# Kernel tuning notes

Measured on AMD Instinct MI355X. Metric: run time of the kernel, lower is better.

## Reference

```python
import jax, jax.numpy as jnp
import numpy as np

N = 100_000      # lidar points (KITTI-scale)
E = 800_000      # knn edges, avg degree 8
C_IN = 4
INTERNAL_H, INTERNAL_W = 240, 1216   # INTERNAL_IMG_SIZE


def setup_inputs() -> dict:
    key = jax.random.key(0)
    ks = jax.random.split(key, 16)
    x = jax.random.normal(ks[0], (N, C_IN), jnp.float32)
    # lidar-like points in velodyne frame: x fwd [5,70], y left [-20,20], z up [-2,1]
    u = jax.random.uniform(ks[1], (N, 3), jnp.float32)
    pos = jnp.stack([5.0 + 65.0 * u[:, 0],
                     -20.0 + 40.0 * u[:, 1],
                     -2.0 + 3.0 * u[:, 2]], axis=1)
    edge_index = jax.random.randint(ks[2], (2, E), 0, N, dtype=jnp.int32)
    batch = jnp.zeros((N,), jnp.int32)
    # folded calibration P2 @ R0 @ Tr: pinhole cam looking down velodyne +x
    f, cx, cy = 720.0, 621.0, 250.0
    proj = jnp.array([[cx, -f, 0.0, 0.0],
                      [cy, 0.0, -f, 0.0],
                      [1.0, 0.0, 0.0, 0.0]], jnp.float32)
    dims = [(C_IN + 3, 64), (64 + 3, 128), (128 + 3, 256)]
    params = {}
    ki = 3
    for li, (din, dout) in enumerate(dims, 1):
        s1, s2 = 1.0 / np.sqrt(din), 1.0 / np.sqrt(dout)
        params[f"w1_{li}"] = jax.random.uniform(ks[ki], (din, dout), jnp.float32, -s1, s1); ki += 1
        params[f"b1_{li}"] = jnp.zeros((dout,), jnp.float32)
        params[f"w2_{li}"] = jax.random.uniform(ks[ki], (dout, dout), jnp.float32, -s2, s2); ki += 1
        params[f"b2_{li}"] = jnp.zeros((dout,), jnp.float32)
    return dict(x=x, pos=pos, edge_index=edge_index, batch=batch, proj=proj,
                img_h=375, img_w=1242, **params)


def _pointnet_conv(x, pos, src, dst, w1, b1, w2, b2):
    # message: local_nn([x_j, pos_j - pos_i]) with MLP = lin1 -> relu -> lin2; aggr = max
    m = jnp.concatenate([x[src], pos[src] - pos[dst]], axis=1)     # [E', din]
    h = jnp.maximum(m @ w1 + b1, 0.0) @ w2 + b2                    # [E', dout]
    return jax.ops.segment_max(h, dst, num_segments=x.shape[0])


def reference(x, pos, edge_index, batch, proj, img_h, img_w,
              w1_1, b1_1, w2_1, b2_1,
              w1_2, b1_2, w2_2, b2_2,
              w1_3, b1_3, w2_3, b2_3):
    n = x.shape[0]
    # PointNetConv adds self-loops by default -> every segment non-empty
    loops = jnp.arange(n, dtype=edge_index.dtype)
    src = jnp.concatenate([edge_index[0], loops])
    dst = jnp.concatenate([edge_index[1], loops])

    h = _pointnet_conv(x, pos, src, dst, w1_1, b1_1, w2_1, b2_1)   # [N, 64]
    h = _pointnet_conv(h, pos, src, dst, w1_2, b1_2, w2_2, b2_2)   # [N, 128]
    h = _pointnet_conv(h, pos, src, dst, w1_3, b1_3, w2_3, b2_3)   # [N, 256]

    # projection: (proj @ [pos; 1]) -> [3, N]; perspective divide; int16 trunc
    hom = proj @ jnp.concatenate([pos.T, jnp.ones((1, n), pos.dtype)], axis=0)
    off_u, off_v = img_w - INTERNAL_W, img_h - INTERNAL_H
    ui = (hom[0] / hom[2]).astype(jnp.int16).astype(jnp.int32) - off_u
    vi = (hom[1] / hom[2]).astype(jnp.int16).astype(jnp.int32) - off_v
    valid = (ui >= 0) & (vi >= 0) & (ui < INTERNAL_W) & (vi < INTERNAL_H)
    # route invalid points out-of-bounds so mode='drop' discards them
    ui = jnp.where(valid, ui, INTERNAL_W)
    vi = jnp.where(valid, vi, INTERNAL_H)

    img = jnp.zeros((1, h.shape[1], INTERNAL_W, INTERNAL_H), h.dtype)  # (B=1, C, 1216, 240)
    img = img.at[0, :, ui, vi].add(h, mode='drop')

    # max_pool2d(kernel=4, stride=4) -> (1, 256, 304, 60)
    B, C, W, H = img.shape
    pooled = img.reshape(B, C, W // 4, 4, H // 4, 4).max(axis=(3, 5))
    return pooled
```

## Files before the change

### kernel.cpp

```cpp
#include <hip/hip_runtime.h>
#include <cstdint>

#define N_PTS 100000
#define N_EDGE 800000
#define N_ITEMS (N_EDGE + N_PTS)
#define IMG_W 1216
#define IMG_H 240
#define OW 304
#define OH 60
#define CHUNK 32
#define BIN_BLOCKS 391

typedef _Float16 f16;
typedef _Float16 f16x8 __attribute__((ext_vector_type(8)));
typedef float f32x4 __attribute__((ext_vector_type(4)));

__device__ __forceinline__ void atomicMaxF(float* addr, float v) {
    if (v >= 0.0f) atomicMax((int*)addr, __float_as_int(v));
    else atomicMin((unsigned int*)addr, __float_as_uint(v));
}

__global__ __launch_bounds__(256)
void init_out_kernel(float* __restrict__ p, long n)
{
    long i = ((long)blockIdx.x * 256 + threadIdx.x) * 4;
    if (i < n) {
        float4 v = {-INFINITY, -INFINITY, -INFINITY, -INFINITY};
        *(float4*)&p[i] = v;
    }
}

template<int DX, int KP, int D>
__global__ __launch_bounds__(256)
void node_mfma_kernel(const float* __restrict__ X, const float* __restrict__ pos,
                      const f16* __restrict__ w1t, const float* __restrict__ b1,
                      f16* __restrict__ A)
{
    constexpr int KB = KP / 32;
    constexpr int NB = D / 16;
    const int tid = threadIdx.x;
    const int wave = tid >> 6;
    const int lane = tid & 63;
    const int row = lane & 15;
    const int kg = lane >> 4;
    const int wbase = (blockIdx.x * 4 + wave) * 32;

    f16x8 pa[2][KB];
#pragma unroll
    for (int mh = 0; mh < 2; ++mh) {
        int n = wbase + mh * 16 + row;
        int ns = (n < N_PTS) ? n : 0;
#pragma unroll
        for (int kb = 0; kb < KB; ++kb) {
            const int c0 = kb * 32 + kg * 8;
            f16x8 h;
#pragma unroll
            for (int j = 0; j < 8; ++j) {
                int k = c0 + j;
                float v = 0.0f;
                if (k < DX) v = X[(long)ns * DX + k];
                else if (k < DX + 3) v = pos[(long)ns * 3 + (k - DX)];
                h[j] = (f16)v;
            }
            pa[mh][kb] = h;
        }
    }

#pragma unroll 2
    for (int nb = 0; nb < NB; ++nb) {
        f32x4 acc0 = {0.0f, 0.0f, 0.0f, 0.0f};
        f32x4 acc1 = {0.0f, 0.0f, 0.0f, 0.0f};
#pragma unroll
        for (int kb = 0; kb < KB; ++kb) {
            f16x8 pb = *(const f16x8*)&w1t[(long)(nb * 16 + row) * KP + kb * 32 + kg * 8];
            acc0 = __builtin_amdgcn_mfma_f32_16x16x32_f16(pa[0][kb], pb, acc0, 0, 0, 0);
            acc1 = __builtin_amdgcn_mfma_f32_16x16x32_f16(pa[1][kb], pb, acc1, 0, 0, 0);
        }
        const int col = nb * 16 + row;
        const float bb = b1[col];
#pragma unroll
        for (int reg = 0; reg < 4; ++reg) {
            int r = kg * 4 + reg;
            int n0 = wbase + r;
            int n1 = wbase + 16 + r;
            if (n0 < N_PTS) A[(long)n0 * D + col] = (f16)(acc0[reg] + bb);
            if (n1 < N_PTS) A[(long)n1 * D + col] = (f16)(acc1[reg] + bb);
        }
    }
}

__global__ void cvt_w1(const float* __restrict__ w1, f16* __restrict__ w1t,
                       int K, int KP, int D)
{
    int i = blockIdx.x * 256 + threadIdx.x;
    if (i >= D * KP) return;
    int c = i / KP, k = i % KP;
    w1t[i] = (k < K) ? (f16)w1[k * D + c] : (f16)0.0f;
}

__global__ void cvt_w2(const float* __restrict__ w2, f16* __restrict__ w2t, int D)
{
    int i = blockIdx.x * 256 + threadIdx.x;
    if (i >= D * D) return;
    int n = i / D, k = i % D;
    w2t[i] = (f16)w2[k * D + n];
}

__global__ void init_hist_kernel(int* __restrict__ hist)
{
    int i = blockIdx.x * 256 + threadIdx.x;
    if (i < N_PTS) hist[i] = 1;
}

__global__ void hist_kernel(const int* __restrict__ ei, int* __restrict__ hist)
{
    int e = blockIdx.x * 256 + threadIdx.x;
    if (e < N_EDGE) atomicAdd(&hist[ei[N_EDGE + e]], 1);
}

__global__ void bsum_kernel(const int* __restrict__ hist, int* __restrict__ bsum)
{
    __shared__ int s[256];
    int i = blockIdx.x * 256 + threadIdx.x;
    s[threadIdx.x] = (i < N_PTS) ? hist[i] : 0;
    __syncthreads();
    for (int off = 128; off > 0; off >>= 1) {
        if (threadIdx.x < off) s[threadIdx.x] += s[threadIdx.x + off];
        __syncthreads();
    }
    if (threadIdx.x == 0) bsum[blockIdx.x] = s[0];
}

__global__ void scan_bsum_kernel(int* __restrict__ bsum)
{
    __shared__ int s[512];
    int t = threadIdx.x;
    int v = (t < BIN_BLOCKS) ? bsum[t] : 0;
    s[t] = v;
    __syncthreads();
    for (int off = 1; off < 512; off <<= 1) {
        int u = (t >= off) ? s[t - off] : 0;
        __syncthreads();
        s[t] += u;
        __syncthreads();
    }
    if (t < BIN_BLOCKS) bsum[t] = s[t] - v;
}

__global__ void rowptr_kernel(const int* __restrict__ hist, const int* __restrict__ bsum,
                              int* __restrict__ woff)
{
    __shared__ int s[256];
    int i = blockIdx.x * 256 + threadIdx.x;
    int v = (i < N_PTS) ? hist[i] : 0;
    s[threadIdx.x] = v;
    __syncthreads();
    for (int off = 1; off < 256; off <<= 1) {
        int u = (threadIdx.x >= off) ? s[threadIdx.x - off] : 0;
        __syncthreads();
        s[threadIdx.x] += u;
        __syncthreads();
    }
    if (i < N_PTS) woff[i] = bsum[blockIdx.x] + s[threadIdx.x] - v;
}

__global__ void scatter_edges_kernel(const int* __restrict__ ei, int* __restrict__ woff,
                                     int* __restrict__ srcS, int* __restrict__ dstS)
{
    int e = blockIdx.x * 256 + threadIdx.x;
    if (e >= N_ITEMS) return;
    int s, d;
    if (e < N_EDGE) { s = ei[e]; d = ei[N_EDGE + e]; }
    else            { s = d = e - N_EDGE; }
    int p = atomicAdd(&woff[d], 1);
    srcS[p] = s;
    dstS[p] = d;
}

template<int D>
__global__ __launch_bounds__(256)
void gemm_msg_kernel(const int* __restrict__ srcA, const int* __restrict__ dstA,
                     const f16* __restrict__ A, const float* __restrict__ pos,
                     const float* __restrict__ w1p, const f16* __restrict__ w2t,
                     const float* __restrict__ b2, float* __restrict__ OUT, int nItems)
{
    constexpr int KB = D / 32;
    constexpr int NB = D / 16;
    const int tid = threadIdx.x;
    const int wave = tid >> 6;
    const int lane = tid & 63;
    const int row = lane & 15;
    const int kg = lane >> 4;
    const long wbase = ((long)blockIdx.x * 4 + wave) * 32;

    int s[2], d[2];
    float px[2], py[2], pz[2];
#pragma unroll
    for (int mh = 0; mh < 2; ++mh) {
        long e = wbase + mh * 16 + row;
        bool ok = (e < nItems);
        int ss = ok ? srcA[e] : 0;
        int dd = ok ? dstA[e] : -1;
        s[mh] = ss; d[mh] = dd;
        int dsafe = ok ? dd : 0;
        px[mh] = pos[(long)dsafe * 3 + 0];
        py[mh] = pos[(long)dsafe * 3 + 1];
        pz[mh] = pos[(long)dsafe * 3 + 2];
    }

    f16x8 pa[2][KB];
#pragma unroll
    for (int kb = 0; kb < KB; ++kb) {
        const int c0 = kb * 32 + kg * 8;
        f16x8 a0 = *(const f16x8*)&A[(long)s[0] * D + c0];
        f16x8 a1 = *(const f16x8*)&A[(long)s[1] * D + c0];
        f16x8 h0, h1;
#pragma unroll
        for (int j = 0; j < 8; ++j) {
            float wx = w1p[c0 + j];
            float wy = w1p[D + c0 + j];
            float wz = w1p[2 * D + c0 + j];
            h0[j] = (f16)fmaxf((float)a0[j] - (px[0] * wx + py[0] * wy + pz[0] * wz), 0.0f);
            h1[j] = (f16)fmaxf((float)a1[j] - (px[1] * wx + py[1] * wy + pz[1] * wz), 0.0f);
        }
        pa[0][kb] = h0;
        pa[1][kb] = h1;
    }

    int dd0[4], dd1[4];
#pragma unroll
    for (int reg = 0; reg < 4; ++reg) {
        int r = kg * 4 + reg;
        dd0[reg] = __shfl(d[0], r);
        dd1[reg] = __shfl(d[1], r);
    }
    bool hd0[4], hd1[4];
    hd0[0] = true; hd1[0] = true;
#pragma unroll
    for (int reg = 1; reg < 4; ++reg) {
        hd0[reg] = (dd0[reg] != dd0[reg - 1]);
        hd1[reg] = (dd1[reg] != dd1[reg - 1]);
    }

#pragma unroll
    for (int nb = 0; nb < NB; ++nb) {
        f32x4 acc0 = {0.0f, 0.0f, 0.0f, 0.0f};
        f32x4 acc1 = {0.0f, 0.0f, 0.0f, 0.0f};
#pragma unroll
        for (int kb = 0; kb < KB; ++kb) {
            f16x8 pb = *(const f16x8*)&w2t[(long)(nb * 16 + row) * D + kb * 32 + kg * 8];
            acc0 = __builtin_amdgcn_mfma_f32_16x16x32_f16(pa[0][kb], pb, acc0, 0, 0, 0);
            acc1 = __builtin_amdgcn_mfma_f32_16x16x32_f16(pa[1][kb], pb, acc1, 0, 0, 0);
        }
        const int col = nb * 16 + row;
        const float bb = b2[col];
        float v0[4], v1[4];
#pragma unroll
        for (int reg = 0; reg < 4; ++reg) { v0[reg] = acc0[reg] + bb; v1[reg] = acc1[reg] + bb; }
        float s0[4], s1[4];
        s0[3] = v0[3]; s1[3] = v1[3];
#pragma unroll
        for (int reg = 2; reg >= 0; --reg) {
            s0[reg] = hd0[reg + 1] ? v0[reg] : fmaxf(v0[reg], s0[reg + 1]);
            s1[reg] = hd1[reg + 1] ? v1[reg] : fmaxf(v1[reg], s1[reg + 1]);
        }
#pragma unroll
        for (int reg = 0; reg < 4; ++reg) {
            if (hd0[reg] && dd0[reg] >= 0) atomicMaxF(&OUT[(long)dd0[reg] * D + col], s0[reg]);
            if (hd1[reg] && dd1[reg] >= 0) atomicMaxF(&OUT[(long)dd1[reg] * D + col], s1[reg]);
        }
    }
}

__global__ void proj_kernel(const float* __restrict__ pos, const float* __restrict__ proj,
                            const int* __restrict__ img_h, const int* __restrict__ img_w,
                            int* __restrict__ pix)
{
    int n = blockIdx.x * blockDim.x + threadIdx.x;
    if (n >= N_PTS) return;
    float px = pos[n * 3 + 0], py = pos[n * 3 + 1], pz = pos[n * 3 + 2];
    float h0 = proj[0] * px + proj[1] * py + proj[2]  * pz + proj[3];
    float h1 = proj[4] * px + proj[5] * py + proj[6]  * pz + proj[7];
    float h2 = proj[8] * px + proj[9] * py + proj[10] * pz + proj[11];
    int off_u = img_w[0] - IMG_W;
    int off_v = img_h[0] - IMG_H;
    int ui = (int)(short)(h0 / h2) - off_u;
    int vi = (int)(short)(h1 / h2) - off_v;
    bool valid = (ui >= 0) && (vi >= 0) && (ui < IMG_W) && (vi < IMG_H);
    pix[n] = valid ? (ui * IMG_H + vi) : -1;
}

__global__ __launch_bounds__(256)
void scatter_kernel(const float* __restrict__ H, const int* __restrict__ pix,
                    float* __restrict__ img, int cbase)
{
    long g = (long)blockIdx.x * blockDim.x + threadIdx.x;
    if (g >= (long)N_PTS * CHUNK) return;
    int n = (int)(g / CHUNK);
    int c = (int)(g % CHUNK);
    int p = pix[n];
    if (p < 0) return;
    atomicAdd(&img[(long)p * CHUNK + c], H[(long)n * 256 + cbase + c]);
}

__global__ __launch_bounds__(CHUNK)
void pool_kernel(const float* __restrict__ img, float* __restrict__ out, int cbase)
{
    int cell = blockIdx.x;
    int wc = cell / OH, hc = cell % OH;
    int c = threadIdx.x;
    float mx = -INFINITY;
#pragma unroll
    for (int i = 0; i < 4; ++i)
#pragma unroll
        for (int j = 0; j < 4; ++j) {
            long p = (long)(wc * 4 + i) * IMG_H + (hc * 4 + j);
            mx = fmaxf(mx, img[p * CHUNK + c]);
        }
    out[(long)(cbase + c) * (OW * OH) + wc * OH + hc] = mx;
}

extern "C" void kernel_launch(void* const* d_in, const int* in_sizes, int n_in,
                              void* d_out, int out_size, void* d_ws, size_t ws_size,
                              hipStream_t stream)
{
    const float* x     = (const float*)d_in[0];
    const float* pos   = (const float*)d_in[1];
    const int*   ei    = (const int*)d_in[2];
    const float* proj  = (const float*)d_in[4];
    const int*   img_h = (const int*)d_in[5];
    const int*   img_w = (const int*)d_in[6];
    const float* w1_1 = (const float*)d_in[7];
    const float* b1_1 = (const float*)d_in[8];
    const float* w2_1 = (const float*)d_in[9];
    const float* b2_1 = (const float*)d_in[10];
    const float* w1_2 = (const float*)d_in[11];
    const float* b1_2 = (const float*)d_in[12];
    const float* w2_2 = (const float*)d_in[13];
    const float* b2_2 = (const float*)d_in[14];
    const float* w1_3 = (const float*)d_in[15];
    const float* b1_3 = (const float*)d_in[16];
    const float* w2_3 = (const float*)d_in[17];
    const float* b2_3 = (const float*)d_in[18];
    float* out = (float*)d_out;

    if (ws_size < 162400000ull) return;
    char* ws = (char*)d_ws;
    float* HH   = (float*)(ws + 0);
    float* F1   = (float*)(ws + 0);
    float* F0   = (float*)(ws + 51200000);
    f16*   A12  = (f16*)(ws + 76800000);
    f16*   A3   = (f16*)(ws + 102400000);
    float* img  = (float*)(ws + 102400000);
    int*   pix  = (int*)(ws + 153600000);
    f16*   w2t3 = (f16*)(ws + 154000000);
    f16*   w2t2 = (f16*)(ws + 154131072);
    f16*   w2t1 = (f16*)(ws + 154163840);
    int*   srcS = (int*)(ws + 154200000);
    int*   dstS = (int*)(ws + 157800000);
    int*   hist = (int*)(ws + 161400000);
    int*   woff = (int*)(ws + 161800000);
    int*   bsum = (int*)(ws + 162200000);
    f16*   w1t3 = (f16*)(ws + 162210000);
    f16*   w1t2 = (f16*)(ws + 162300000);
    f16*   w1t1 = (f16*)(ws + 162330000);

    const int NODE_BLOCKS = (N_PTS + 127) / 128;
    const int EDGE_BLOCKS = (N_ITEMS + 127) / 128;
    const int E256  = (N_EDGE + 255) / 256;
    const int I256  = (N_ITEMS + 255) / 256;

    init_hist_kernel<<<BIN_BLOCKS, 256, 0, stream>>>(hist);
    hist_kernel<<<E256, 256, 0, stream>>>(ei, hist);
    bsum_kernel<<<BIN_BLOCKS, 256, 0, stream>>>(hist, bsum);
    scan_bsum_kernel<<<1, 512, 0, stream>>>(bsum);
    rowptr_kernel<<<BIN_BLOCKS, 256, 0, stream>>>(hist, bsum, woff);
    scatter_edges_kernel<<<I256, 256, 0, stream>>>(ei, woff, srcS, dstS);

    cvt_w1<<<(64 * 32 + 255) / 256, 256, 0, stream>>>(w1_1, w1t1, 7, 32, 64);
    cvt_w1<<<(128 * 96 + 255) / 256, 256, 0, stream>>>(w1_2, w1t2, 67, 96, 128);
    cvt_w1<<<(256 * 160 + 255) / 256, 256, 0, stream>>>(w1_3, w1t3, 131, 160, 256);
    cvt_w2<<<(64 * 64 + 255) / 256, 256, 0, stream>>>(w2_1, w2t1, 64);
    cvt_w2<<<(128 * 128 + 255) / 256, 256, 0, stream>>>(w2_2, w2t2, 128);
    cvt_w2<<<(256 * 256 + 255) / 256, 256, 0, stream>>>(w2_3, w2t3, 256);
    proj_kernel<<<(N_PTS + 255) / 256, 256, 0, stream>>>(pos, proj, img_h, img_w, pix);
    init_out_kernel<<<(N_PTS * 64 / 4 + 255) / 256, 256, 0, stream>>>(F0, (long)N_PTS * 64);
    init_out_kernel<<<(N_PTS * 128 / 4 + 255) / 256, 256, 0, stream>>>(F1, (long)N_PTS * 128);

    node_mfma_kernel<4, 32, 64><<<NODE_BLOCKS, 256, 0, stream>>>(x, pos, w1t1, b1_1, A12);
    gemm_msg_kernel<64><<<EDGE_BLOCKS, 256, 0, stream>>>(srcS, dstS, A12, pos, w1_1 + 4 * 64, w2t1, b2_1, F0, N_ITEMS);

    node_mfma_kernel<64, 96, 128><<<NODE_BLOCKS, 256, 0, stream>>>(F0, pos, w1t2, b1_2, A12);
    gemm_msg_kernel<128><<<EDGE_BLOCKS, 256, 0, stream>>>(srcS, dstS, A12, pos, w1_2 + 64 * 128, w2t2, b2_2, F1, N_ITEMS);

    node_mfma_kernel<128, 160, 256><<<NODE_BLOCKS, 256, 0, stream>>>(F1, pos, w1t3, b1_3, A3);
    init_out_kernel<<<(N_PTS * 256 / 4 + 255) / 256, 256, 0, stream>>>(HH, (long)N_PTS * 256);
    gemm_msg_kernel<256><<<EDGE_BLOCKS, 256, 0, stream>>>(srcS, dstS, A3, pos, w1_3 + 128 * 256, w2t3, b2_3, HH, N_ITEMS);

    for (int cb = 0; cb < 256; cb += CHUNK) {
        hipMemsetAsync(img, 0, (size_t)IMG_W * IMG_H * CHUNK * 4, stream);
        scatter_kernel<<<(N_PTS * CHUNK) / 256, 256, 0, stream>>>(HH, pix, img, cb);
        pool_kernel<<<OW * OH, CHUNK, 0, stream>>>(img, out, cb);
    }
}
```

Baseline: 1.787 ms.

## Pad CSR segments to 16-row windows so each MFMA tile maps to one destination

Each destination's edge list is padded to a multiple of 16 by duplicating the self-loop source, and a per-window destination table is built. Every MFMA 16-row tile then belongs to a single node. The max reduction becomes a cross-lane shuffle plus one store per column, and the atomic is used only when a node spans more than one window. This removes the per-edge dstS array, the segmented scan and most of the atomics. The cost is extra padded rows of GEMM work, and the launch always covers a fixed WIN_MAX window count, with empty windows exiting early.

```diff
diff --git a/kernel.cpp b/kernel.cpp
--- a/kernel.cpp
+++ b/kernel.cpp
@@ -4,6 +4,7 @@
 #define N_PTS 100000
 #define N_EDGE 800000
 #define N_ITEMS (N_EDGE + N_PTS)
+#define WIN_MAX 150000
 #define IMG_W 1216
 #define IMG_H 240
 #define OW 304
@@ -122,7 +123,7 @@
 {
     __shared__ int s[256];
     int i = blockIdx.x * 256 + threadIdx.x;
-    s[threadIdx.x] = (i < N_PTS) ? hist[i] : 0;
+    s[threadIdx.x] = (i < N_PTS) ? ((hist[i] + 15) & ~15) : 0;
     __syncthreads();
     for (int off = 128; off > 0; off >>= 1) {
         if (threadIdx.x < off) s[threadIdx.x] += s[threadIdx.x + off];
@@ -148,11 +149,11 @@
 }
 
 __global__ void rowptr_kernel(const int* __restrict__ hist, const int* __restrict__ bsum,
-                              int* __restrict__ woff)
+                              int* __restrict__ woff, int* __restrict__ rbeg)
 {
     __shared__ int s[256];
     int i = blockIdx.x * 256 + threadIdx.x;
-    int v = (i < N_PTS) ? hist[i] : 0;
+    int v = (i < N_PTS) ? ((hist[i] + 15) & ~15) : 0;
     s[threadIdx.x] = v;
     __syncthreads();
     for (int off = 1; off < 256; off <<= 1) {
@@ -161,11 +162,15 @@
         s[threadIdx.x] += u;
         __syncthreads();
     }
-    if (i < N_PTS) woff[i] = bsum[blockIdx.x] + s[threadIdx.x] - v;
+    if (i < N_PTS) {
+        int st = bsum[blockIdx.x] + s[threadIdx.x] - v;
+        woff[i] = st;
+        rbeg[i] = st;
+    }
 }
 
 __global__ void scatter_edges_kernel(const int* __restrict__ ei, int* __restrict__ woff,
-                                     int* __restrict__ srcS, int* __restrict__ dstS)
+                                     int* __restrict__ srcS)
 {
     int e = blockIdx.x * 256 + threadIdx.x;
     if (e >= N_ITEMS) return;
@@ -174,15 +179,30 @@
     else            { s = d = e - N_EDGE; }
     int p = atomicAdd(&woff[d], 1);
     srcS[p] = s;
-    dstS[p] = d;
+}
+
+__global__ void fill_pad_kernel(const int* __restrict__ hist, const int* __restrict__ rbeg,
+                                const int* __restrict__ woff, int* __restrict__ srcS,
+                                int* __restrict__ dstW)
+{
+    int i = blockIdx.x * 256 + threadIdx.x;
+    if (i >= N_PTS) return;
+    int begin = rbeg[i];
+    int padl = (hist[i] + 15) & ~15;
+    int endp = begin + padl;
+    for (int p = woff[i]; p < endp; ++p) srcS[p] = i;
+    int nw = padl >> 4;
+    int w0 = begin >> 4;
+    int flag = (nw > 1) ? 1 : 0;
+    for (int w = 0; w < nw; ++w) dstW[w0 + w] = (i << 1) | flag;
 }
 
 template<int D>
 __global__ __launch_bounds__(256)
-void gemm_msg_kernel(const int* __restrict__ srcA, const int* __restrict__ dstA,
+void gemm_win_kernel(const int* __restrict__ srcS, const int* __restrict__ dstW,
                      const f16* __restrict__ A, const float* __restrict__ pos,
                      const float* __restrict__ w1p, const f16* __restrict__ w2t,
-                     const float* __restrict__ b2, float* __restrict__ OUT, int nItems)
+                     const float* __restrict__ b2, float* __restrict__ OUT)
 {
     constexpr int KB = D / 32;
     constexpr int NB = D / 16;
@@ -191,55 +211,38 @@
     const int lane = tid & 63;
     const int row = lane & 15;
     const int kg = lane >> 4;
-    const long wbase = ((long)blockIdx.x * 4 + wave) * 32;
-
-    int s[2], d[2];
-    float px[2], py[2], pz[2];
+    const int w0 = (blockIdx.x * 4 + wave) * 2;
+
+    const int dwa = dstW[w0];
+    const int dwb = dstW[w0 + 1];
+    if (dwa < 0 && dwb < 0) return;
+    const int dA = dwa >> 1, dB = dwb >> 1;
+
+    f16x8 pa[2][KB];
+    const int dw2[2] = {dwa, dwb};
+    const int dd2[2] = {dA, dB};
 #pragma unroll
     for (int mh = 0; mh < 2; ++mh) {
-        long e = wbase + mh * 16 + row;
-        bool ok = (e < nItems);
-        int ss = ok ? srcA[e] : 0;
-        int dd = ok ? dstA[e] : -1;
-        s[mh] = ss; d[mh] = dd;
-        int dsafe = ok ? dd : 0;
-        px[mh] = pos[(long)dsafe * 3 + 0];
-        py[mh] = pos[(long)dsafe * 3 + 1];
-        pz[mh] = pos[(long)dsafe * 3 + 2];
-    }
-
-    f16x8 pa[2][KB];
-#pragma unroll
-    for (int kb = 0; kb < KB; ++kb) {
-        const int c0 = kb * 32 + kg * 8;
-        f16x8 a0 = *(const f16x8*)&A[(long)s[0] * D + c0];
-        f16x8 a1 = *(const f16x8*)&A[(long)s[1] * D + c0];
-        f16x8 h0, h1;
-#pragma unroll
-        for (int j = 0; j < 8; ++j) {
-            float wx = w1p[c0 + j];
-            float wy = w1p[D + c0 + j];
-            float wz = w1p[2 * D + c0 + j];
-            h0[j] = (f16)fmaxf((float)a0[j] - (px[0] * wx + py[0] * wy + pz[0] * wz), 0.0f);
-            h1[j] = (f16)fmaxf((float)a1[j] - (px[1] * wx + py[1] * wy + pz[1] * wz), 0.0f);
-        }
-        pa[0][kb] = h0;
-        pa[1][kb] = h1;
-    }
-
-    int dd0[4], dd1[4];
-#pragma unroll
-    for (int reg = 0; reg < 4; ++reg) {
-        int r = kg * 4 + reg;
-        dd0[reg] = __shfl(d[0], r);
-        dd1[reg] = __shfl(d[1], r);
-    }
-    bool hd0[4], hd1[4];
-    hd0[0] = true; hd1[0] = true;
-#pragma unroll
-    for (int reg = 1; reg < 4; ++reg) {
-        hd0[reg] = (dd0[reg] != dd0[reg - 1]);
-        hd1[reg] = (dd1[reg] != dd1[reg - 1]);
+        const bool ok = (dw2[mh] >= 0);
+        const int ds = ok ? dd2[mh] : 0;
+        const float qx = pos[(long)ds * 3 + 0];
+        const float qy = pos[(long)ds * 3 + 1];
+        const float qz = pos[(long)ds * 3 + 2];
+        const int s = ok ? srcS[(w0 + mh) * 16 + row] : 0;
+#pragma unroll
+        for (int kb = 0; kb < KB; ++kb) {
+            const int c0 = kb * 32 + kg * 8;
+            f16x8 a = *(const f16x8*)&A[(long)s * D + c0];
+            f16x8 h;
+#pragma unroll
+            for (int j = 0; j < 8; ++j) {
+                float wx = w1p[c0 + j];
+                float wy = w1p[D + c0 + j];
+                float wz = w1p[2 * D + c0 + j];
+                h[j] = (f16)fmaxf((float)a[j] - (qx * wx + qy * wy + qz * wz), 0.0f);
+            }
+            pa[mh][kb] = h;
+        }
     }
 
 #pragma unroll
@@ -254,20 +257,23 @@
         }
         const int col = nb * 16 + row;
         const float bb = b2[col];
-        float v0[4], v1[4];
-#pragma unroll
-        for (int reg = 0; reg < 4; ++reg) { v0[reg] = acc0[reg] + bb; v1[reg] = acc1[reg] + bb; }
-        float s0[4], s1[4];
-        s0[3] = v0[3]; s1[3] = v1[3];
-#pragma unroll
-        for (int reg = 2; reg >= 0; --reg) {
-            s0[reg] = hd0[reg + 1] ? v0[reg] : fmaxf(v0[reg], s0[reg + 1]);
-            s1[reg] = hd1[reg + 1] ? v1[reg] : fmaxf(v1[reg], s1[reg + 1]);
-        }
-#pragma unroll
-        for (int reg = 0; reg < 4; ++reg) {
-            if (hd0[reg] && dd0[reg] >= 0) atomicMaxF(&OUT[(long)dd0[reg] * D + col], s0[reg]);
-            if (hd1[reg] && dd1[reg] >= 0) atomicMaxF(&OUT[(long)dd1[reg] * D + col], s1[reg]);
+        float m0 = fmaxf(fmaxf(acc0[0], acc0[1]), fmaxf(acc0[2], acc0[3]));
+        float m1 = fmaxf(fmaxf(acc1[0], acc1[1]), fmaxf(acc1[2], acc1[3]));
+        m0 = fmaxf(m0, __shfl_xor(m0, 16));
+        m0 = fmaxf(m0, __shfl_xor(m0, 32));
+        m1 = fmaxf(m1, __shfl_xor(m1, 16));
+        m1 = fmaxf(m1, __shfl_xor(m1, 32));
+        if (kg == 0) {
+            if (dwa >= 0) {
+                float v = m0 + bb;
+                if (dwa & 1) atomicMaxF(&OUT[(long)dA * D + col], v);
+                else OUT[(long)dA * D + col] = v;
+            }
+            if (dwb >= 0) {
+                float v = m1 + bb;
+                if (dwb & 1) atomicMaxF(&OUT[(long)dB * D + col], v);
+                else OUT[(long)dB * D + col] = v;
+            }
         }
     }
 }
@@ -344,7 +350,7 @@
     const float* b2_3 = (const float*)d_in[18];
     float* out = (float*)d_out;
 
-    if (ws_size < 162400000ull) return;
+    if (ws_size < 165800000ull) return;
     char* ws = (char*)d_ws;
     float* HH   = (float*)(ws + 0);
     float* F1   = (float*)(ws + 0);
@@ -357,16 +363,17 @@
     f16*   w2t2 = (f16*)(ws + 154131072);
     f16*   w2t1 = (f16*)(ws + 154163840);
     int*   srcS = (int*)(ws + 154200000);
-    int*   dstS = (int*)(ws + 157800000);
-    int*   hist = (int*)(ws + 161400000);
-    int*   woff = (int*)(ws + 161800000);
-    int*   bsum = (int*)(ws + 162200000);
-    f16*   w1t3 = (f16*)(ws + 162210000);
-    f16*   w1t2 = (f16*)(ws + 162300000);
-    f16*   w1t1 = (f16*)(ws + 162330000);
+    int*   hist = (int*)(ws + 163800000);
+    int*   woff = (int*)(ws + 164200000);
+    int*   rbeg = (int*)(ws + 164600000);
+    int*   bsum = (int*)(ws + 165000000);
+    int*   dstW = (int*)(ws + 165004096);
+    f16*   w1t3 = (f16*)(ws + 165610000);
+    f16*   w1t2 = (f16*)(ws + 165700000);
+    f16*   w1t1 = (f16*)(ws + 165730000);
 
     const int NODE_BLOCKS = (N_PTS + 127) / 128;
-    const int EDGE_BLOCKS = (N_ITEMS + 127) / 128;
+    const int WIN_BLOCKS  = WIN_MAX / 8;
     const int E256  = (N_EDGE + 255) / 256;
     const int I256  = (N_ITEMS + 255) / 256;
 
@@ -374,8 +381,10 @@
     hist_kernel<<<E256, 256, 0, stream>>>(ei, hist);
     bsum_kernel<<<BIN_BLOCKS, 256, 0, stream>>>(hist, bsum);
     scan_bsum_kernel<<<1, 512, 0, stream>>>(bsum);
-    rowptr_kernel<<<BIN_BLOCKS, 256, 0, stream>>>(hist, bsum, woff);
-    scatter_edges_kernel<<<I256, 256, 0, stream>>>(ei, woff, srcS, dstS);
+    rowptr_kernel<<<BIN_BLOCKS, 256, 0, stream>>>(hist, bsum, woff, rbeg);
+    scatter_edges_kernel<<<I256, 256, 0, stream>>>(ei, woff, srcS);
+    hipMemsetAsync(dstW, 0xFF, WIN_MAX * 4, stream);
+    fill_pad_kernel<<<BIN_BLOCKS, 256, 0, stream>>>(hist, rbeg, woff, srcS, dstW);
 
     cvt_w1<<<(64 * 32 + 255) / 256, 256, 0, stream>>>(w1_1, w1t1, 7, 32, 64);
     cvt_w1<<<(128 * 96 + 255) / 256, 256, 0, stream>>>(w1_2, w1t2, 67, 96, 128);
@@ -388,14 +397,14 @@
     init_out_kernel<<<(N_PTS * 128 / 4 + 255) / 256, 256, 0, stream>>>(F1, (long)N_PTS * 128);
 
     node_mfma_kernel<4, 32, 64><<<NODE_BLOCKS, 256, 0, stream>>>(x, pos, w1t1, b1_1, A12);
-    gemm_msg_kernel<64><<<EDGE_BLOCKS, 256, 0, stream>>>(srcS, dstS, A12, pos, w1_1 + 4 * 64, w2t1, b2_1, F0, N_ITEMS);
+    gemm_win_kernel<64><<<WIN_BLOCKS, 256, 0, stream>>>(srcS, dstW, A12, pos, w1_1 + 4 * 64, w2t1, b2_1, F0);
 
     node_mfma_kernel<64, 96, 128><<<NODE_BLOCKS, 256, 0, stream>>>(F0, pos, w1t2, b1_2, A12);
-    gemm_msg_kernel<128><<<EDGE_BLOCKS, 256, 0, stream>>>(srcS, dstS, A12, pos, w1_2 + 64 * 128, w2t2, b2_2, F1, N_ITEMS);
+    gemm_win_kernel<128><<<WIN_BLOCKS, 256, 0, stream>>>(srcS, dstW, A12, pos, w1_2 + 64 * 128, w2t2, b2_2, F1);
 
     node_mfma_kernel<128, 160, 256><<<NODE_BLOCKS, 256, 0, stream>>>(F1, pos, w1t3, b1_3, A3);
     init_out_kernel<<<(N_PTS * 256 / 4 + 255) / 256, 256, 0, stream>>>(HH, (long)N_PTS * 256);
-    gemm_msg_kernel<256><<<EDGE_BLOCKS, 256, 0, stream>>>(srcS, dstS, A3, pos, w1_3 + 128 * 256, w2t3, b2_3, HH, N_ITEMS);
+    gemm_win_kernel<256><<<WIN_BLOCKS, 256, 0, stream>>>(srcS, dstW, A3, pos, w1_3 + 128 * 256, w2t3, b2_3, HH);
 
     for (int cb = 0; cb < 256; cb += CHUNK) {
         hipMemsetAsync(img, 0, (size_t)IMG_W * IMG_H * CHUNK * 4, stream);
```

Measured after the change: 1.887 ms. 5.6% more time.
